# Performance work log

Measured on AMD Instinct MI355X. Metric: run time of the kernel, lower is better.

The kernel has to match this reference:

```python
import jax, jax.numpy as jnp
import numpy as np

HEADS = 4

def _unfold3x3(x):
    # x: [N, C, H, W] -> [N, C*9, H*W], channel-slowest / kernel-fastest (matches torch F.unfold)
    N, C, H, W = x.shape
    p = jnp.pad(x, ((0, 0), (0, 0), (1, 1), (1, 1)))
    pats = jnp.stack([p[:, :, i:i + H, j:j + W] for i in range(3) for j in range(3)], axis=2)
    return pats.reshape(N, C * 9, H * W)

def _conv1x1(x, w):
    # x: [N, Cin, H, W], w: [Cout, Cin]
    return jnp.einsum('nchw,oc->nohw', x, w)

def _dwconv3x3(x, w):
    # depthwise 3x3, x: [N, C, H, W], w: [C, 1, 3, 3]
    return jax.lax.conv_general_dilated(
        x, w, window_strides=(1, 1), padding='SAME',
        feature_group_count=x.shape[1],
        dimension_numbers=('NCHW', 'OIHW', 'NCHW'))

def _layernorm(x, w, b, eps=1e-5):
    m = jnp.mean(x, axis=-1, keepdims=True)
    v = jnp.mean(jnp.square(x - m), axis=-1, keepdims=True)
    return (x - m) * jax.lax.rsqrt(v + eps) * w + b

def _l2norm(x, eps=1e-12):
    n = jnp.sqrt(jnp.sum(jnp.square(x), axis=-1, keepdims=True))
    return x / jnp.maximum(n, eps)

def setup_inputs() -> dict:
    key = jax.random.key(0)
    ks = jax.random.split(key, 12)
    channels, angRes, h, w, b = 64, 5, 32, 32, 1
    a = angRes * angRes
    D = channels * 2          # 128
    hid = int(D * 2.66)       # 340
    s = 0.02
    return {
        'buffer': jax.random.normal(ks[0], (b, channels, a, h, w), jnp.float32),
        'mlp_w': jax.random.normal(ks[1], (D, channels * 9), jnp.float32) * s,
        'ln_attn_w': jnp.ones((D,), jnp.float32),
        'ln_attn_b': jnp.zeros((D,), jnp.float32),
        'ln_ffn_w': jnp.ones((D,), jnp.float32),
        'ln_ffn_b': jnp.zeros((D,), jnp.float32),
        'qkv_w': jax.random.normal(ks[2], (3 * D, D), jnp.float32) * s,
        'qkv_dw_w': jax.random.normal(ks[3], (3 * D, 1, 3, 3), jnp.float32) * s,
        'temperature': jnp.ones((HEADS, 1, 1), jnp.float32),
        'proj_attn_w': jax.random.normal(ks[4], (D, D), jnp.float32) * s,
        'ffn_in_w': jax.random.normal(ks[5], (2 * hid, D), jnp.float32) * s,
        'ffn_dw_w': jax.random.normal(ks[6], (2 * hid, 1, 3, 3), jnp.float32) * s,
        'ffn_out_w': jax.random.normal(ks[7], (D, hid), jnp.float32) * s,
        'proj3d_w': jax.random.normal(ks[8], (channels, D), jnp.float32) * s,
    }

def reference(buffer, mlp_w, ln_attn_w, ln_attn_b, ln_ffn_w, ln_ffn_b,
              qkv_w, qkv_dw_w, temperature, proj_attn_w,
              ffn_in_w, ffn_dw_w, ffn_out_w, proj3d_w):
    b, c, a, h, w = buffer.shape
    N, D = b * a, mlp_w.shape[0]
    L = h * w
    cph = D // HEADS

    # SAI2Token: [b,c,a,h,w] -> [(b a),c,h,w] -> unfold -> [L, N, c*9] -> MLP -> [L, N, D]
    buf2d = buffer.transpose(0, 2, 1, 3, 4).reshape(N, c, h, w)
    tok = _unfold3x3(buf2d).transpose(2, 0, 1)          # [L, N, c*9]
    tok = tok @ mlp_w.T                                  # [L, N, D]

    # --- attention branch ---
    tn = _layernorm(tok, ln_attn_w, ln_attn_b)
    x = tn.transpose(1, 2, 0).reshape(N, D, h, w)        # '(h w) n d -> n d h w'
    qkv = _dwconv3x3(_conv1x1(x, qkv_w), qkv_dw_w)       # [N, 3D, h, w]
    q, k, v = jnp.split(qkv, 3, axis=1)

    def heads(t):  # 'n (head c) h w -> n head (h w) c'
        return t.reshape(N, HEADS, cph, L).transpose(0, 1, 3, 2)
    q, k, v = heads(q), heads(k), heads(v)
    q, k = _l2norm(q), _l2norm(k)
    attn = jnp.einsum('nhlc,nhmc->nhlm', q, k) * temperature  # [N, HEADS, L, L]
    attn = jax.nn.softmax(attn, axis=-1)
    out = jnp.einsum('nhlm,nhmc->nhlc', attn, v)         # [N, HEADS, L, cph]
    out = out.transpose(0, 1, 3, 2).reshape(N, D, h, w)
    out = _conv1x1(out, proj_attn_w)
    tok = tok + out.reshape(N, D, L).transpose(2, 0, 1)

    # --- GDFN branch ---
    tf = _layernorm(tok, ln_ffn_w, ln_ffn_b)
    x2 = tf.transpose(1, 2, 0).reshape(N, D, h, w)
    y = _dwconv3x3(_conv1x1(x2, ffn_in_w), ffn_dw_w)     # [N, 2*hid, h, w]
    y1, y2 = jnp.split(y, 2, axis=1)
    y = jax.nn.gelu(y1, approximate=False) * y2
    y = _conv1x1(y, ffn_out_w)                           # [N, D, h, w]
    tok = tok + y.reshape(N, D, L).transpose(2, 0, 1)

    # Token2SAI: '(h w) (b a) d -> b d a h w' then 1x1x1 conv3d
    x5 = tok.reshape(h, w, b, a, D).transpose(2, 4, 3, 0, 1)  # [b, D, a, h, w]
    out = jnp.einsum('bdahw,od->boahw', x5, proj3d_w)
    return out
```

## Files before the change

kernel.cpp:

```cpp
#include <hip/hip_runtime.h>
#include <math.h>

#define M_TOK 25600

typedef __attribute__((ext_vector_type(8))) short bf16x8;
typedef __attribute__((ext_vector_type(4))) float f32x4;
typedef __attribute__((ext_vector_type(4))) int   i32x4;
typedef __attribute__((ext_vector_type(2))) int   i32x2;

__device__ __forceinline__ unsigned short f2b(float x) {
    unsigned u = __builtin_bit_cast(unsigned, x);
    return (unsigned short)((u + 0x7fffu + ((u >> 16) & 1u)) >> 16);
}
__device__ __forceinline__ float b2f(unsigned short h) {
    unsigned u = ((unsigned)h) << 16;
    return __builtin_bit_cast(float, u);
}
__device__ __forceinline__ unsigned cvtpk(float lo, float hi) {
    unsigned r;
    asm("v_cvt_pk_bf16_f32 %0, %1, %2" : "=v"(r) : "v"(lo), "v"(hi));
    return r;
}

__global__ __launch_bounds__(256) void prep_k(const float* __restrict__ s0, const float* __restrict__ s1,
                                              const float* __restrict__ s2, const float* __restrict__ s3,
                                              const float* __restrict__ s4, const float* __restrict__ s5,
                                              const float* __restrict__ qw, const float* __restrict__ fw,
                                              short* __restrict__ dst,
                                              float* __restrict__ wqT, float* __restrict__ wgT) {
    int i = blockIdx.x * 256 + threadIdx.x;
    if (i >= 297320) return;
    if (i < 287744) {
        if (i < 81920) {
            int r = i % 640, d = i / 640;
            int tap = r >> 6, cc = r & 63;
            dst[i] = (tap < 9) ? (short)f2b(s0[(d * 64 + cc) * 9 + tap]) : (short)0;
            return;
        }
        if (i >= 234496 && i < 279552) {
            int l = i - 234496;
            int row = l / 352, col = l % 352;
            dst[i] = (col < 340) ? (short)f2b(s4[row * 340 + col]) : (short)0;
            return;
        }
        const float* s; int off;
        if      (i < 131072) { s = s1; off = i - 81920; }
        else if (i < 147456) { s = s2; off = i - 131072; }
        else if (i < 234496) { s = s3; off = i - 147456; }
        else                 { s = s5; off = i - 279552; }
        dst[i] = (short)f2b(s[off]);
        return;
    }
    int j = i - 287744;
    if (j < 3456) {
        int tap = j / 384, c = j % 384;
        wqT[j] = qw[c * 9 + tap];
    } else {
        int k = j - 3456;
        int tap = k / 680, c = k % 680;
        wgT[k] = fw[c * 9 + tap];
    }
}

template <bool ADD, bool TROUT, bool AF32>
__global__ __launch_bounds__(256) void mm64_k(const void* __restrict__ Avp,
                                              const short* __restrict__ W,
                                              float* __restrict__ outp,
                                              int M, int N, int K) {
    __shared__ __align__(16) short As[2][64 * 40];
    __shared__ __align__(16) short Bs[2][64 * 40];
    const int tid = threadIdx.x;
    const int bm = blockIdx.x * 64;
    const int bn = blockIdx.y * 64;
    const int w = tid >> 6, lane = tid & 63;
    const int h = lane >> 4, l15 = lane & 15;
    const int wm = (w >> 1) * 32, wn = (w & 1) * 32;

    const int row = tid >> 2, c4 = tid & 3;
    const int gnW = bn + row;

    f32x4 acc[2][2];
#pragma unroll
    for (int i = 0; i < 2; ++i)
#pragma unroll
        for (int j = 0; j < 2; ++j) acc[i][j] = (f32x4){0.f, 0.f, 0.f, 0.f};

    short av[8], wv[8];

    auto ldA = [&](int k0, short* tmp) {
        int gk = k0 + c4 * 8;
        size_t abase = (size_t)(bm + row) * K + gk;
        if (AF32) {
            const float* ap = (const float*)Avp + abase;
            float4 va = *(const float4*)ap;
            float4 vb = *(const float4*)(ap + 4);
            tmp[0] = (short)f2b(va.x); tmp[1] = (short)f2b(va.y);
            tmp[2] = (short)f2b(va.z); tmp[3] = (short)f2b(va.w);
            tmp[4] = (short)f2b(vb.x); tmp[5] = (short)f2b(vb.y);
            tmp[6] = (short)f2b(vb.z); tmp[7] = (short)f2b(vb.w);
        } else {
            const short* ap = (const short*)Avp + abase;
            i32x2 a = *(const i32x2*)ap;
            i32x2 b = *(const i32x2*)(ap + 4);
            *(i32x2*)&tmp[0] = a; *(i32x2*)&tmp[4] = b;
        }
    };
    auto ldW = [&](int k0, short* tmp) {
        const short* wp = W + (size_t)gnW * K + k0 + c4 * 8;
        i32x2 a = *(const i32x2*)wp;
        i32x2 b = *(const i32x2*)(wp + 4);
        *(i32x2*)&tmp[0] = a; *(i32x2*)&tmp[4] = b;
    };

    ldA(0, av);
    ldW(0, wv);

    int ph = 0;
    for (int k0 = 0; k0 < K; k0 += 32, ph ^= 1) {
        *(i32x4*)&As[ph][row * 40 + c4 * 8] = *(i32x4*)av;
        *(i32x4*)&Bs[ph][row * 40 + c4 * 8] = *(i32x4*)wv;
        if (k0 + 32 < K) {
            ldA(k0 + 32, av);
            ldW(k0 + 32, wv);
        }
        __syncthreads();

        bf16x8 af[2], bf[2];
#pragma unroll
        for (int mi = 0; mi < 2; ++mi) af[mi] = *(const bf16x8*)&As[ph][(wm + mi * 16 + l15) * 40 + h * 8];
#pragma unroll
        for (int nj = 0; nj < 2; ++nj) bf[nj] = *(const bf16x8*)&Bs[ph][(wn + nj * 16 + l15) * 40 + h * 8];
#pragma unroll
        for (int mi = 0; mi < 2; ++mi)
#pragma unroll
            for (int nj = 0; nj < 2; ++nj) {
                if (TROUT)
                    acc[mi][nj] = __builtin_amdgcn_mfma_f32_16x16x32_bf16(bf[nj], af[mi], acc[mi][nj], 0, 0, 0);
                else
                    acc[mi][nj] = __builtin_amdgcn_mfma_f32_16x16x32_bf16(af[mi], bf[nj], acc[mi][nj], 0, 0, 0);
            }
    }

    if (!TROUT) {
#pragma unroll
        for (int mi = 0; mi < 2; ++mi) {
#pragma unroll
            for (int nj = 0; nj < 2; ++nj) {
                int gn = bn + wn + nj * 16 + l15;
#pragma unroll
                for (int r = 0; r < 4; ++r) {
                    int gm = bm + wm + mi * 16 + h * 4 + r;
                    size_t oi = (size_t)gm * N + gn;
                    if (ADD) outp[oi] += acc[mi][nj][r];
                    else     outp[oi] = acc[mi][nj][r];
                }
            }
        }
    } else {
#pragma unroll
        for (int mi = 0; mi < 2; ++mi) {
            int gm = bm + wm + mi * 16 + l15;
#pragma unroll
            for (int nj = 0; nj < 2; ++nj)
#pragma unroll
                for (int r = 0; r < 4; ++r) {
                    int gn = bn + wn + nj * 16 + h * 4 + r;
                    outp[(size_t)gn * M + gm] = acc[mi][nj][r];
                }
        }
    }
}

__global__ __launch_bounds__(256) void mmim_k(const float* __restrict__ buf,
                                              const short* __restrict__ W,
                                              float* __restrict__ outp) {
    const int N = 128, K = 640;
    __shared__ __align__(16) short As[2][128 * 40];
    __shared__ __align__(16) short Bs[2][64 * 40];
    const int tid = threadIdx.x;
    const int bm = blockIdx.x * 128;
    const int bn = blockIdx.y * 64;
    const int w = tid >> 6, lane = tid & 63;
    const int h = lane >> 4, l15 = lane & 15;
    const int wm = (w >> 1) * 64, wn = (w & 1) * 32;

    const int rowA0 = tid >> 2, c4 = tid & 3;
    const int rowA1 = rowA0 + 64;
    const int gnW = bn + rowA0;

    f32x4 acc[4][2];
#pragma unroll
    for (int i = 0; i < 4; ++i)
#pragma unroll
        for (int j = 0; j < 2; ++j) acc[i][j] = (f32x4){0.f, 0.f, 0.f, 0.f};

    auto ldA = [&](int row, int k0, short* tmp) {
        int t = bm + row;
        int l = t & 1023, n = t >> 10;
        int y = l >> 5, x = l & 31;
        int k = k0 + c4 * 8;
        int tap = k >> 6, cc0 = k & 63;
        bool ok = (tap < 9);
        int ti = 0, tj = 0;
        if (ok) { ti = tap / 3; tj = tap - ti * 3; }
        int yy = y + ti - 1, xx = x + tj - 1;
        ok = ok && (yy >= 0) && (yy < 32) && (xx >= 0) && (xx < 32);
        if (ok) {
            const float* bp = buf + (size_t)cc0 * M_TOK + (n << 10) + (yy << 5) + xx;
#pragma unroll
            for (int i = 0; i < 8; ++i) tmp[i] = (short)f2b(bp[(size_t)i * M_TOK]);
        } else {
#pragma unroll
            for (int i = 0; i < 8; ++i) tmp[i] = 0;
        }
    };
    auto ldW = [&](int k0, short* tmp) {
        const short* wp = W + (size_t)gnW * K + k0 + c4 * 8;
        i32x2 a = *(const i32x2*)wp;
        i32x2 b = *(const i32x2*)(wp + 4);
        *(i32x2*)&tmp[0] = a; *(i32x2*)&tmp[4] = b;
    };
    auto compute = [&](int ph) {
        bf16x8 af[4], bf[2];
#pragma unroll
        for (int mi = 0; mi < 4; ++mi) af[mi] = *(const bf16x8*)&As[ph][(wm + mi * 16 + l15) * 40 + h * 8];
#pragma unroll
        for (int nj = 0; nj < 2; ++nj) bf[nj] = *(const bf16x8*)&Bs[ph][(wn + nj * 16 + l15) * 40 + h * 8];
#pragma unroll
        for (int mi = 0; mi < 4; ++mi)
#pragma unroll
            for (int nj = 0; nj < 2; ++nj)
                acc[mi][nj] = __builtin_amdgcn_mfma_f32_16x16x32_bf16(af[mi], bf[nj], acc[mi][nj], 0, 0, 0);
    };

    short a0A[8], a1A[8], wvA[8];
    short a0B[8], a1B[8], wvB[8];
    ldA(rowA0, 0, a0A);  ldA(rowA1, 0, a1A);  ldW(0, wvA);
    ldA(rowA0, 32, a0B); ldA(rowA1, 32, a1B); ldW(32, wvB);

    for (int k0 = 0; k0 < K; k0 += 64) {
        *(i32x4*)&As[0][rowA0 * 40 + c4 * 8] = *(i32x4*)a0A;
        *(i32x4*)&As[0][rowA1 * 40 + c4 * 8] = *(i32x4*)a1A;
        *(i32x4*)&Bs[0][rowA0 * 40 + c4 * 8] = *(i32x4*)wvA;
        if (k0 + 64 < K) { ldA(rowA0, k0 + 64, a0A); ldA(rowA1, k0 + 64, a1A); ldW(k0 + 64, wvA); }
        __syncthreads();
        compute(0);
        *(i32x4*)&As[1][rowA0 * 40 + c4 * 8] = *(i32x4*)a0B;
        *(i32x4*)&As[1][rowA1 * 40 + c4 * 8] = *(i32x4*)a1B;
        *(i32x4*)&Bs[1][rowA0 * 40 + c4 * 8] = *(i32x4*)wvB;
        if (k0 + 96 < K) { ldA(rowA0, k0 + 96, a0B); ldA(rowA1, k0 + 96, a1B); ldW(k0 + 96, wvB); }
        __syncthreads();
        compute(1);
    }

#pragma unroll
    for (int mi = 0; mi < 4; ++mi) {
#pragma unroll
        for (int nj = 0; nj < 2; ++nj) {
            int gn = bn + wn + nj * 16 + l15;
#pragma unroll
            for (int r = 0; r < 4; ++r) {
                int gm = bm + wm + mi * 16 + h * 4 + r;
                outp[(size_t)gm * N + gn] = acc[mi][nj][r];
            }
        }
    }
}

__global__ __launch_bounds__(256) void mmw_k(const short* __restrict__ A,
                                             const short* __restrict__ W,
                                             short* __restrict__ outp,
                                             int M, int N, int K) {
    __shared__ __align__(16) short As[2][128 * 40];
    __shared__ __align__(16) short Bs[2][128 * 40];
    const int tid = threadIdx.x;
    const int bm = blockIdx.x * 128;
    const int bn = blockIdx.y * 128;
    const int w = tid >> 6, lane = tid & 63;
    const int h = lane >> 4, l15 = lane & 15;
    const int wm = (w >> 1) * 64, wn = (w & 1) * 64;

    const int row0 = tid >> 2, c4 = tid & 3;
    const int row1 = row0 + 64;

    f32x4 acc[4][4];
#pragma unroll
    for (int i = 0; i < 4; ++i)
#pragma unroll
        for (int j = 0; j < 4; ++j) acc[i][j] = (f32x4){0.f, 0.f, 0.f, 0.f};

    auto ldA = [&](int row, int k0, short* tmp) {
        const short* ap = A + (size_t)(bm + row) * K + k0 + c4 * 8;
        i32x2 x = *(const i32x2*)ap;
        i32x2 y = *(const i32x2*)(ap + 4);
        *(i32x2*)&tmp[0] = x; *(i32x2*)&tmp[4] = y;
    };
    auto ldW = [&](int row, int k0, short* tmp) {
        int gn = bn + row;
        if (gn < N) {
            const short* wp = W + (size_t)gn * K + k0 + c4 * 8;
            i32x2 x = *(const i32x2*)wp;
            i32x2 y = *(const i32x2*)(wp + 4);
            *(i32x2*)&tmp[0] = x; *(i32x2*)&tmp[4] = y;
        } else {
#pragma unroll
            for (int i = 0; i < 8; ++i) tmp[i] = 0;
        }
    };
    auto compute = [&](int ph) {
        bf16x8 af[4], bf[4];
#pragma unroll
        for (int mi = 0; mi < 4; ++mi) af[mi] = *(const bf16x8*)&As[ph][(wm + mi * 16 + l15) * 40 + h * 8];
#pragma unroll
        for (int nj = 0; nj < 4; ++nj) bf[nj] = *(const bf16x8*)&Bs[ph][(wn + nj * 16 + l15) * 40 + h * 8];
#pragma unroll
        for (int mi = 0; mi < 4; ++mi)
#pragma unroll
            for (int nj = 0; nj < 4; ++nj)
                acc[mi][nj] = __builtin_amdgcn_mfma_f32_16x16x32_bf16(af[mi], bf[nj], acc[mi][nj], 0, 0, 0);
    };

    short a0A[8], a1A[8], b0A[8], b1A[8];
    short a0B[8], a1B[8], b0B[8], b1B[8];
    ldA(row0, 0, a0A);  ldA(row1, 0, a1A);  ldW(row0, 0, b0A);  ldW(row1, 0, b1A);
    ldA(row0, 32, a0B); ldA(row1, 32, a1B); ldW(row0, 32, b0B); ldW(row1, 32, b1B);

    for (int k0 = 0; k0 < K; k0 += 64) {
        *(i32x4*)&As[0][row0 * 40 + c4 * 8] = *(i32x4*)a0A;
        *(i32x4*)&As[0][row1 * 40 + c4 * 8] = *(i32x4*)a1A;
        *(i32x4*)&Bs[0][row0 * 40 + c4 * 8] = *(i32x4*)b0A;
        *(i32x4*)&Bs[0][row1 * 40 + c4 * 8] = *(i32x4*)b1A;
        if (k0 + 64 < K) {
            ldA(row0, k0 + 64, a0A); ldA(row1, k0 + 64, a1A);
            ldW(row0, k0 + 64, b0A); ldW(row1, k0 + 64, b1A);
        }
        __syncthreads();
        compute(0);
        *(i32x4*)&As[1][row0 * 40 + c4 * 8] = *(i32x4*)a0B;
        *(i32x4*)&As[1][row1 * 40 + c4 * 8] = *(i32x4*)a1B;
        *(i32x4*)&Bs[1][row0 * 40 + c4 * 8] = *(i32x4*)b0B;
        *(i32x4*)&Bs[1][row1 * 40 + c4 * 8] = *(i32x4*)b1B;
        if (k0 + 96 < K) {
            ldA(row0, k0 + 96, a0B); ldA(row1, k0 + 96, a1B);
            ldW(row0, k0 + 96, b0B); ldW(row1, k0 + 96, b1B);
        }
        __syncthreads();
        compute(1);
    }

#pragma unroll
    for (int mi = 0; mi < 4; ++mi) {
#pragma unroll
        for (int nj = 0; nj < 4; ++nj) {
            int gn = bn + wn + nj * 16 + l15;
            if (gn < N) {
#pragma unroll
                for (int r = 0; r < 4; ++r) {
                    int gm = bm + wm + mi * 16 + h * 4 + r;
                    outp[(size_t)gm * N + gn] = (short)f2b(acc[mi][nj][r]);
                }
            }
        }
    }
}

__global__ __launch_bounds__(256) void ln_k(const float* __restrict__ in,
                                            const float* __restrict__ w,
                                            const float* __restrict__ b,
                                            short* __restrict__ out) {
    int t = blockIdx.x * 4 + (threadIdx.x >> 6);
    int lane = threadIdx.x & 63;
    float2 v = *(const float2*)(in + (size_t)t * 128 + lane * 2);
    float s = v.x + v.y, sq = v.x * v.x + v.y * v.y;
#pragma unroll
    for (int off = 32; off > 0; off >>= 1) { s += __shfl_xor(s, off); sq += __shfl_xor(sq, off); }
    float mean = s * (1.f / 128.f);
    float var = sq * (1.f / 128.f) - mean * mean;
    float rstd = rsqrtf(var + 1e-5f);
    float2 wv = *(const float2*)(w + lane * 2);
    float2 bv = *(const float2*)(b + lane * 2);
    float ox = (v.x - mean) * rstd * wv.x + bv.x;
    float oy = (v.y - mean) * rstd * wv.y + bv.y;
    ((unsigned*)out)[(size_t)t * 64 + lane] = f2b(ox) | ((unsigned)f2b(oy) << 16);
}

__global__ __launch_bounds__(256) void dwl2n_k(const short* __restrict__ in,
                                               const float* __restrict__ wqT,
                                               const float* __restrict__ temp,
                                               short* __restrict__ out) {
    int idx = blockIdx.x * 256 + threadIdx.x;
    int q = idx % 48;
    int t = idx / 48;
    int c0 = q * 8;
    int l = t & 1023, n = t >> 10;
    int y = l >> 5, x = l & 31;
    int tb = n << 10;

    float acc[8];
#pragma unroll
    for (int k = 0; k < 8; ++k) acc[k] = 0.f;

#pragma unroll
    for (int i = 0; i < 3; ++i) {
        int yy = y + i - 1;
        if (yy < 0 || yy >= 32) continue;
#pragma unroll
        for (int j = 0; j < 3; ++j) {
            int xx = x + j - 1;
            if (xx < 0 || xx >= 32) continue;
            bf16x8 d = *(const bf16x8*)(in + (size_t)(tb + (yy << 5) + xx) * 384 + c0);
            float4 wa = *(const float4*)(wqT + (i * 3 + j) * 384 + c0);
            float4 wb = *(const float4*)(wqT + (i * 3 + j) * 384 + c0 + 4);
            acc[0] += b2f((unsigned short)d[0]) * wa.x;
            acc[1] += b2f((unsigned short)d[1]) * wa.y;
            acc[2] += b2f((unsigned short)d[2]) * wa.z;
            acc[3] += b2f((unsigned short)d[3]) * wa.w;
            acc[4] += b2f((unsigned short)d[4]) * wb.x;
            acc[5] += b2f((unsigned short)d[5]) * wb.y;
            acc[6] += b2f((unsigned short)d[6]) * wb.z;
            acc[7] += b2f((unsigned short)d[7]) * wb.w;
        }
    }
    float ss = 0.f;
#pragma unroll
    for (int k = 0; k < 8; ++k) ss += acc[k] * acc[k];
    ss += __shfl_xor(ss, 1);
    ss += __shfl_xor(ss, 2);
    float sc;
    if (c0 < 128)       sc = (1.f / fmaxf(sqrtf(ss), 1e-12f)) * temp[c0 >> 5] * 1.44269504089f;
    else if (c0 < 256)  sc = 1.f / fmaxf(sqrtf(ss), 1e-12f);
    else                sc = 1.f;
    unsigned o[4];
#pragma unroll
    for (int k = 0; k < 4; ++k)
        o[k] = f2b(acc[2 * k] * sc) | ((unsigned)f2b(acc[2 * k + 1] * sc) << 16);
    *(i32x4*)(out + (size_t)t * 384 + c0) = *(i32x4*)o;
}

__global__ __launch_bounds__(256) void gdfn2_k(const short* __restrict__ in,
                                               const float* __restrict__ wgT,
                                               short* __restrict__ out) {
    int idx = blockIdx.x * 256 + threadIdx.x;
    int q = idx % 44;
    int t = idx / 44;
    int c0 = q * 8;
    short* op = out + (size_t)t * 352 + c0;
    if (q == 43) {
        *(i32x4*)op = (i32x4){0, 0, 0, 0};
        return;
    }
    int l = t & 1023, n = t >> 10;
    int y = l >> 5, x = l & 31;
    int tb = n << 10;

    float a[8], g[8];
#pragma unroll
    for (int k = 0; k < 8; ++k) { a[k] = 0.f; g[k] = 0.f; }

#pragma unroll
    for (int i = 0; i < 3; ++i) {
        int yy = y + i - 1;
        if (yy < 0 || yy >= 32) continue;
#pragma unroll
        for (int j = 0; j < 3; ++j) {
            int xx = x + j - 1;
            if (xx < 0 || xx >= 32) continue;
            const short* p = in + (size_t)(tb + (yy << 5) + xx) * 680 + c0;
            bf16x8 d1 = *(const bf16x8*)p;
            i32x2 d2a = *(const i32x2*)(p + 340);
            i32x2 d2b = *(const i32x2*)(p + 344);
            short d2[8];
            *(i32x2*)&d2[0] = d2a; *(i32x2*)&d2[4] = d2b;
            const float* wp = wgT + (i * 3 + j) * 680 + c0;
            float4 w1a = *(const float4*)wp;
            float4 w1b = *(const float4*)(wp + 4);
            float w1[8] = {w1a.x, w1a.y, w1a.z, w1a.w, w1b.x, w1b.y, w1b.z, w1b.w};
            float w2[8];
#pragma unroll
            for (int k = 0; k < 8; ++k) w2[k] = wp[340 + k];
#pragma unroll
            for (int k = 0; k < 8; ++k) {
                a[k] += b2f((unsigned short)d1[k]) * w1[k];
                g[k] += b2f((unsigned short)d2[k]) * w2[k];
            }
        }
    }
    unsigned o[4];
#pragma unroll
    for (int k = 0; k < 4; ++k) {
        float r0 = 0.5f * a[2 * k] * (1.f + erff(a[2 * k] * 0.70710678118f)) * g[2 * k];
        float r1 = 0.5f * a[2 * k + 1] * (1.f + erff(a[2 * k + 1] * 0.70710678118f)) * g[2 * k + 1];
        o[k] = f2b(r0) | ((unsigned)f2b(r1) << 16);
    }
    if (q == 42) { o[2] = 0; o[3] = 0; }
    *(i32x4*)op = *(i32x4*)o;
}

__global__ __launch_bounds__(256) void attn_k(const short* __restrict__ qkv,
                                              short* __restrict__ outp) {
    __shared__ __align__(16) short Ks[2][64 * 40];
    __shared__ __align__(16) short Vp[2][2048];
    const int b = blockIdx.x;
    const int orig = (b & 7) * 200 + (b >> 3);
    const int qt = orig & 15, nh = orig >> 4;
    const int hd = nh & 3, n = nh >> 2;
    const int tid = threadIdx.x;
    const int w = tid >> 6, lane = tid & 63;
    const int h = lane >> 4, l15 = lane & 15;
    const size_t base = (size_t)n * 1024 * 384;
    const int qrow = qt * 64 + w * 16 + l15;

    bf16x8 qf = *(const bf16x8*)(qkv + base + (size_t)qrow * 384 + hd * 32 + h * 8);
    f32x4 o0 = {0.f,0.f,0.f,0.f}, o1 = {0.f,0.f,0.f,0.f};
    f32x4 osum = {0.f,0.f,0.f,0.f};
    union { unsigned u[4]; bf16x8 v; } ones;
#pragma unroll
    for (int r = 0; r < 4; ++r) ones.u[r] = 0x3F803F80u;

    const int skey = tid >> 2, sc4 = tid & 3;
    const int sg = skey >> 5, skey5 = skey & 31;
    const int sh = (skey5 >> 2) & 3;
    const int sj = (skey5 & 3) + ((skey5 >> 4) << 2);
    const int sgran0 = (sg * 4 + sh) * 32 + sc4 * 8;
    const short* kbase = qkv + base + (size_t)skey * 384 + 128 + hd * 32 + sc4 * 8;

    auto scatterV = [&](int nb, i32x4 vreg) {
        short vs[8];
        *(i32x4*)vs = vreg;
#pragma unroll
        for (int i = 0; i < 8; ++i) {
            int gran = sgran0 + i;
            gran ^= (gran >> 3) & 7;
            Vp[nb][gran * 8 + sj] = vs[i];
        }
    };
    auto compute = [&](int nb) {
        const bf16x8 kf0 = *(const bf16x8*)&Ks[nb][l15 * 40 + h * 8];
        const bf16x8 kf1 = *(const bf16x8*)&Ks[nb][(16 + l15) * 40 + h * 8];
        const bf16x8 kf2 = *(const bf16x8*)&Ks[nb][(32 + l15) * 40 + h * 8];
        const bf16x8 kf3 = *(const bf16x8*)&Ks[nb][(48 + l15) * 40 + h * 8];
        int gr0 = h * 32 + l15;            gr0 ^= (gr0 >> 3) & 7;
        int gr1 = h * 32 + 16 + l15;       gr1 ^= (gr1 >> 3) & 7;
        int gr2 = (4 + h) * 32 + l15;      gr2 ^= (gr2 >> 3) & 7;
        int gr3 = (4 + h) * 32 + 16 + l15; gr3 ^= (gr3 >> 3) & 7;
        const bf16x8 va0 = *(const bf16x8*)&Vp[nb][gr0 * 8];
        const bf16x8 va1 = *(const bf16x8*)&Vp[nb][gr1 * 8];
        const bf16x8 vb0 = *(const bf16x8*)&Vp[nb][gr2 * 8];
        const bf16x8 vb1 = *(const bf16x8*)&Vp[nb][gr3 * 8];
        const f32x4 z = {0.f, 0.f, 0.f, 0.f};

        f32x4 s0 = __builtin_amdgcn_mfma_f32_16x16x32_bf16(kf0, qf, z, 0, 0, 0);
        f32x4 s1 = __builtin_amdgcn_mfma_f32_16x16x32_bf16(kf1, qf, z, 0, 0, 0);
        f32x4 s2 = __builtin_amdgcn_mfma_f32_16x16x32_bf16(kf2, qf, z, 0, 0, 0);
        f32x4 s3 = __builtin_amdgcn_mfma_f32_16x16x32_bf16(kf3, qf, z, 0, 0, 0);
        float p[16];
#pragma unroll
        for (int r = 0; r < 4; ++r) {
            p[r]      = exp2f(s0[r]);
            p[4 + r]  = exp2f(s1[r]);
            p[8 + r]  = exp2f(s2[r]);
            p[12 + r] = exp2f(s3[r]);
        }
        union { unsigned u[4]; bf16x8 v; } pf1, pf2;
#pragma unroll
        for (int r = 0; r < 4; ++r) {
            pf1.u[r] = cvtpk(p[2 * r], p[2 * r + 1]);
            pf2.u[r] = cvtpk(p[8 + 2 * r], p[8 + 2 * r + 1]);
        }
        osum = __builtin_amdgcn_mfma_f32_16x16x32_bf16(ones.v, pf1.v, osum, 0, 0, 0);
        osum = __builtin_amdgcn_mfma_f32_16x16x32_bf16(ones.v, pf2.v, osum, 0, 0, 0);
        o0 = __builtin_amdgcn_mfma_f32_16x16x32_bf16(va0, pf1.v, o0, 0, 0, 0);
        o1 = __builtin_amdgcn_mfma_f32_16x16x32_bf16(va1, pf1.v, o1, 0, 0, 0);
        o0 = __builtin_amdgcn_mfma_f32_16x16x32_bf16(vb0, pf2.v, o0, 0, 0, 0);
        o1 = __builtin_amdgcn_mfma_f32_16x16x32_bf16(vb1, pf2.v, o1, 0, 0, 0);
    };

    i32x4 kregA = *(const i32x4*)kbase;
    i32x4 vregA = *(const i32x4*)(kbase + 128);
    i32x4 kregB = *(const i32x4*)(kbase + (size_t)64 * 384);
    i32x4 vregB = *(const i32x4*)(kbase + (size_t)64 * 384 + 128);

    for (int t = 0; t < 16; t += 2) {
        *(i32x4*)&Ks[0][skey * 40 + sc4 * 8] = kregA;
        scatterV(0, vregA);
        if (t + 2 < 16) {
            const short* kp = kbase + (size_t)(t + 2) * 64 * 384;
            kregA = *(const i32x4*)kp;
            vregA = *(const i32x4*)(kp + 128);
        }
        __syncthreads();
        compute(0);
        *(i32x4*)&Ks[1][skey * 40 + sc4 * 8] = kregB;
        scatterV(1, vregB);
        if (t + 3 < 16) {
            const short* kp = kbase + (size_t)(t + 3) * 64 * 384;
            kregB = *(const i32x4*)kp;
            vregB = *(const i32x4*)(kp + 128);
        }
        __syncthreads();
        compute(1);
    }

    float inv = 1.f / osum[0];

    size_t ob = ((size_t)n * 1024 + qrow) * 128 + hd * 32;
    unsigned u;
    u = f2b(o0[0] * inv) | ((unsigned)f2b(o0[1] * inv) << 16); *(unsigned*)(outp + ob + h * 4) = u;
    u = f2b(o0[2] * inv) | ((unsigned)f2b(o0[3] * inv) << 16); *(unsigned*)(outp + ob + h * 4 + 2) = u;
    u = f2b(o1[0] * inv) | ((unsigned)f2b(o1[1] * inv) << 16); *(unsigned*)(outp + ob + 16 + h * 4) = u;
    u = f2b(o1[2] * inv) | ((unsigned)f2b(o1[3] * inv) << 16); *(unsigned*)(outp + ob + 16 + h * 4 + 2) = u;
}

extern "C" void kernel_launch(void* const* d_in, const int* in_sizes, int n_in,
                              void* d_out, int out_size, void* d_ws, size_t ws_size,
                              hipStream_t stream) {
    const float* buffer      = (const float*)d_in[0];
    const float* mlp_w       = (const float*)d_in[1];
    const float* ln_attn_w   = (const float*)d_in[2];
    const float* ln_attn_b   = (const float*)d_in[3];
    const float* ln_ffn_w    = (const float*)d_in[4];
    const float* ln_ffn_b    = (const float*)d_in[5];
    const float* qkv_w       = (const float*)d_in[6];
    const float* qkv_dw_w    = (const float*)d_in[7];
    const float* temperature = (const float*)d_in[8];
    const float* proj_attn_w = (const float*)d_in[9];
    const float* ffn_in_w    = (const float*)d_in[10];
    const float* ffn_dw_w    = (const float*)d_in[11];
    const float* ffn_out_w   = (const float*)d_in[12];
    const float* proj3d_w    = (const float*)d_in[13];

    char* wsb = (char*)d_ws;
    short* Wbf     = (short*)wsb;
    short* mlpW    = Wbf;
    short* qkvW    = Wbf + 81920;
    short* projW   = Wbf + 131072;
    short* ffnInW  = Wbf + 147456;
    short* ffnOutW = Wbf + 234496;
    short* p3dW    = Wbf + 279552;
    float* wqT     = (float*)(wsb + 575488);
    float* wgT     = (float*)(wsb + 589312);
    float* tok     = (float*)(wsb + 33381792);
    short* LNbf    = (short*)(wsb + 46488992);
    short* QKVpre  = (short*)(wsb + 53042592);
    short* qkvb    = (short*)(wsb + 72703392);
    short* AObf    = (short*)(wsb + 92364192);
    short* F1      = (short*)(wsb + 98917792);
    short* G       = (short*)(wsb + 133733792);

    dim3 blk(256);

    prep_k<<<1162, blk, 0, stream>>>(mlp_w, qkv_w, proj_attn_w, ffn_in_w, ffn_out_w, proj3d_w,
                                     qkv_dw_w, ffn_dw_w, Wbf, wqT, wgT);

    mmim_k<<<dim3(200, 2), blk, 0, stream>>>(buffer, mlpW, tok);
    ln_k<<<6400, blk, 0, stream>>>(tok, ln_attn_w, ln_attn_b, LNbf);
    mmw_k<<<dim3(200, 3), blk, 0, stream>>>(LNbf, qkvW, QKVpre, M_TOK, 384, 128);
    dwl2n_k<<<4800, blk, 0, stream>>>(QKVpre, wqT, temperature, qkvb);
    attn_k<<<1600, blk, 0, stream>>>(qkvb, AObf);
    mm64_k<true, false, false><<<dim3(400, 2), blk, 0, stream>>>(AObf, projW, tok, M_TOK, 128, 128);
    ln_k<<<6400, blk, 0, stream>>>(tok, ln_ffn_w, ln_ffn_b, LNbf);
    mmw_k<<<dim3(200, 6), blk, 0, stream>>>(LNbf, ffnInW, F1, M_TOK, 680, 128);
    gdfn2_k<<<4400, blk, 0, stream>>>(F1, wgT, G);
    mm64_k<true, false, false><<<dim3(400, 2), blk, 0, stream>>>(G, ffnOutW, tok, M_TOK, 128, 352);
    mm64_k<false, true, true><<<dim3(400, 1), blk, 0, stream>>>(tok, p3dW, (float*)d_out, M_TOK, 64, 128);
}
```

Before: 201.1 us.

## Split attention keys in halves across blocks and combine partials in new kernel

Splits the 1024-key attention loop into two halves handled by separate blocks, doubling the grid to 3200 blocks. Each half writes unnormalized fp32 outputs and partial softmax sums, and a new comb_k kernel adds them and normalizes to bf16. It also wraps the MFMA groups in s_setprio to favor matrix issue. The aim is more parallelism and shorter per-block serial loops, at the cost of an extra launch and fp32 partial-result traffic that reuses the F1 workspace region.

```diff
diff --git a/kernel.cpp b/kernel.cpp
--- a/kernel.cpp
+++ b/kernel.cpp
@@ -497,12 +497,15 @@
 }
 
 __global__ __launch_bounds__(256) void attn_k(const short* __restrict__ qkv,
-                                              short* __restrict__ outp) {
+                                              float* __restrict__ AOf,
+                                              float* __restrict__ PS) {
     __shared__ __align__(16) short Ks[2][64 * 40];
     __shared__ __align__(16) short Vp[2][2048];
     const int b = blockIdx.x;
-    const int orig = (b & 7) * 200 + (b >> 3);
-    const int qt = orig & 15, nh = orig >> 4;
+    const int orig = (b & 7) * 400 + (b >> 3);
+    const int kh = orig & 1;
+    const int rest = orig >> 1;
+    const int qt = rest & 15, nh = rest >> 4;
     const int hd = nh & 3, n = nh >> 2;
     const int tid = threadIdx.x;
     const int w = tid >> 6, lane = tid & 63;
@@ -522,7 +525,7 @@
     const int sh = (skey5 >> 2) & 3;
     const int sj = (skey5 & 3) + ((skey5 >> 4) << 2);
     const int sgran0 = (sg * 4 + sh) * 32 + sc4 * 8;
-    const short* kbase = qkv + base + (size_t)skey * 384 + 128 + hd * 32 + sc4 * 8;
+    const short* kbase = qkv + base + (size_t)(kh * 512 + skey) * 384 + 128 + hd * 32 + sc4 * 8;
 
     auto scatterV = [&](int nb, i32x4 vreg) {
         short vs[8];
@@ -549,10 +552,12 @@
         const bf16x8 vb1 = *(const bf16x8*)&Vp[nb][gr3 * 8];
         const f32x4 z = {0.f, 0.f, 0.f, 0.f};
 
+        __builtin_amdgcn_s_setprio(1);
         f32x4 s0 = __builtin_amdgcn_mfma_f32_16x16x32_bf16(kf0, qf, z, 0, 0, 0);
         f32x4 s1 = __builtin_amdgcn_mfma_f32_16x16x32_bf16(kf1, qf, z, 0, 0, 0);
         f32x4 s2 = __builtin_amdgcn_mfma_f32_16x16x32_bf16(kf2, qf, z, 0, 0, 0);
         f32x4 s3 = __builtin_amdgcn_mfma_f32_16x16x32_bf16(kf3, qf, z, 0, 0, 0);
+        __builtin_amdgcn_s_setprio(0);
         float p[16];
 #pragma unroll
         for (int r = 0; r < 4; ++r) {
@@ -567,12 +572,14 @@
             pf1.u[r] = cvtpk(p[2 * r], p[2 * r + 1]);
             pf2.u[r] = cvtpk(p[8 + 2 * r], p[8 + 2 * r + 1]);
         }
+        __builtin_amdgcn_s_setprio(1);
         osum = __builtin_amdgcn_mfma_f32_16x16x32_bf16(ones.v, pf1.v, osum, 0, 0, 0);
         osum = __builtin_amdgcn_mfma_f32_16x16x32_bf16(ones.v, pf2.v, osum, 0, 0, 0);
         o0 = __builtin_amdgcn_mfma_f32_16x16x32_bf16(va0, pf1.v, o0, 0, 0, 0);
         o1 = __builtin_amdgcn_mfma_f32_16x16x32_bf16(va1, pf1.v, o1, 0, 0, 0);
         o0 = __builtin_amdgcn_mfma_f32_16x16x32_bf16(vb0, pf2.v, o0, 0, 0, 0);
         o1 = __builtin_amdgcn_mfma_f32_16x16x32_bf16(vb1, pf2.v, o1, 0, 0, 0);
+        __builtin_amdgcn_s_setprio(0);
     };
 
     i32x4 kregA = *(const i32x4*)kbase;
@@ -580,10 +587,10 @@
     i32x4 kregB = *(const i32x4*)(kbase + (size_t)64 * 384);
     i32x4 vregB = *(const i32x4*)(kbase + (size_t)64 * 384 + 128);
 
-    for (int t = 0; t < 16; t += 2) {
+    for (int t = 0; t < 8; t += 2) {
         *(i32x4*)&Ks[0][skey * 40 + sc4 * 8] = kregA;
         scatterV(0, vregA);
-        if (t + 2 < 16) {
+        if (t + 2 < 8) {
             const short* kp = kbase + (size_t)(t + 2) * 64 * 384;
             kregA = *(const i32x4*)kp;
             vregA = *(const i32x4*)(kp + 128);
@@ -592,7 +599,7 @@
         compute(0);
         *(i32x4*)&Ks[1][skey * 40 + sc4 * 8] = kregB;
         scatterV(1, vregB);
-        if (t + 3 < 16) {
+        if (t + 3 < 8) {
             const short* kp = kbase + (size_t)(t + 3) * 64 * 384;
             kregB = *(const i32x4*)kp;
             vregB = *(const i32x4*)(kp + 128);
@@ -601,14 +608,33 @@
         compute(1);
     }
 
-    float inv = 1.f / osum[0];
-
     size_t ob = ((size_t)n * 1024 + qrow) * 128 + hd * 32;
-    unsigned u;
-    u = f2b(o0[0] * inv) | ((unsigned)f2b(o0[1] * inv) << 16); *(unsigned*)(outp + ob + h * 4) = u;
-    u = f2b(o0[2] * inv) | ((unsigned)f2b(o0[3] * inv) << 16); *(unsigned*)(outp + ob + h * 4 + 2) = u;
-    u = f2b(o1[0] * inv) | ((unsigned)f2b(o1[1] * inv) << 16); *(unsigned*)(outp + ob + 16 + h * 4) = u;
-    u = f2b(o1[2] * inv) | ((unsigned)f2b(o1[3] * inv) << 16); *(unsigned*)(outp + ob + 16 + h * 4 + 2) = u;
+    float* dst = AOf + (size_t)kh * (M_TOK * 128) + ob;
+    *(float4*)(dst + h * 4)      = (float4){o0[0], o0[1], o0[2], o0[3]};
+    *(float4*)(dst + 16 + h * 4) = (float4){o1[0], o1[1], o1[2], o1[3]};
+    if (h == 0)
+        PS[(size_t)kh * (M_TOK * 4) + ((size_t)n * 1024 + qrow) * 4 + hd] = osum[0];
+}
+
+__global__ __launch_bounds__(256) void comb_k(const float* __restrict__ AOf,
+                                              const float* __restrict__ PS,
+                                              short* __restrict__ out) {
+    int idx = blockIdx.x * 256 + threadIdx.x;
+    int g = idx & 15;
+    int t = idx >> 4;
+    int c0 = g * 8;
+    const float* p0 = AOf + (size_t)t * 128 + c0;
+    const float* p1 = p0 + (size_t)M_TOK * 128;
+    int hd = c0 >> 5;
+    float inv = 1.f / (PS[(size_t)t * 4 + hd] + PS[(size_t)M_TOK * 4 + (size_t)t * 4 + hd]);
+    float4 a0 = *(const float4*)p0, a1 = *(const float4*)(p0 + 4);
+    float4 b0 = *(const float4*)p1, b1 = *(const float4*)(p1 + 4);
+    unsigned o[4];
+    o[0] = f2b((a0.x + b0.x) * inv) | ((unsigned)f2b((a0.y + b0.y) * inv) << 16);
+    o[1] = f2b((a0.z + b0.z) * inv) | ((unsigned)f2b((a0.w + b0.w) * inv) << 16);
+    o[2] = f2b((a1.x + b1.x) * inv) | ((unsigned)f2b((a1.y + b1.y) * inv) << 16);
+    o[3] = f2b((a1.z + b1.z) * inv) | ((unsigned)f2b((a1.w + b1.w) * inv) << 16);
+    *(i32x4*)(out + (size_t)t * 128 + c0) = *(i32x4*)o;
 }
 
 extern "C" void kernel_launch(void* const* d_in, const int* in_sizes, int n_in,
@@ -646,6 +672,8 @@
     short* AObf    = (short*)(wsb + 92364192);
     short* F1      = (short*)(wsb + 98917792);
     short* G       = (short*)(wsb + 133733792);
+    float* AOf     = (float*)(wsb + 98917792);
+    float* PSb     = (float*)(wsb + 125132192);
 
     dim3 blk(256);
 
@@ -656,7 +684,8 @@
     ln_k<<<6400, blk, 0, stream>>>(tok, ln_attn_w, ln_attn_b, LNbf);
     mmw_k<<<dim3(200, 3), blk, 0, stream>>>(LNbf, qkvW, QKVpre, M_TOK, 384, 128);
     dwl2n_k<<<4800, blk, 0, stream>>>(QKVpre, wqT, temperature, qkvb);
-    attn_k<<<1600, blk, 0, stream>>>(qkvb, AObf);
+    attn_k<<<3200, blk, 0, stream>>>(qkvb, AOf, PSb);
+    comb_k<<<1600, blk, 0, stream>>>(AOf, PSb, AObf);
     mm64_k<true, false, false><<<dim3(400, 2), blk, 0, stream>>>(AObf, projW, tok, M_TOK, 128, 128);
     ln_k<<<6400, blk, 0, stream>>>(tok, ln_ffn_w, ln_ffn_b, LNbf);
     mmw_k<<<dim3(200, 6), blk, 0, stream>>>(LNbf, ffnInW, F1, M_TOK, 680, 128);
```

After: 207.0 us. 1.03x slower.
